# Optimization experiments

Hardware: AMD Instinct MI355X
Metric: run time of the kernel (lower is better)

## Reference

```python
import jax, jax.numpy as jnp
import numpy as np

B, T, HID = 2, 2048, 2048
NH, NKV, HD = 16, 4, 128
GROUPS = NH // NKV

def _rotate_half(t):
    t1, t2 = jnp.split(t, 2, axis=-1)
    return jnp.concatenate([-t2, t1], axis=-1)

def _apply_rotary(t, cos, sin):
    # t: [B, H, T, D], cos/sin: [1, 1, T, D]
    return t * cos + _rotate_half(t) * sin

def setup_inputs() -> dict:
    key = jax.random.key(0)
    ks = jax.random.split(key, 6)
    x = jax.random.normal(ks[0], (B, T, HID), dtype=jnp.float32)
    # real rotary tables
    inv_freq = 1.0 / (10000.0 ** (jnp.arange(0, HD, 2, dtype=jnp.float32) / HD))
    pos = jnp.arange(T, dtype=jnp.float32)
    freqs = jnp.outer(pos, inv_freq)            # [T, D/2]
    emb = jnp.concatenate([freqs, freqs], -1)   # [T, D]
    cos = jnp.cos(emb)[None, None]              # [1,1,T,D]
    sin = jnp.sin(emb)[None, None]
    s = 0.02
    Wq = jax.random.normal(ks[1], (HID, NH * HD), dtype=jnp.float32) * s
    Wk = jax.random.normal(ks[2], (HID, NKV * HD), dtype=jnp.float32) * s
    Wv = jax.random.normal(ks[3], (HID, NKV * HD), dtype=jnp.float32) * s
    Wo = jax.random.normal(ks[4], (NH * HD, HID), dtype=jnp.float32) * s
    return {"x": x, "cos": cos, "sin": sin, "Wq": Wq, "Wk": Wk, "Wv": Wv, "Wo": Wo}

def reference(x, cos, sin, Wq, Wk, Wv, Wo):
    b, t, _ = x.shape
    q = (x @ Wq).reshape(b, t, NH, HD).transpose(0, 2, 1, 3)    # [B,NH,T,D]
    k = (x @ Wk).reshape(b, t, NKV, HD).transpose(0, 2, 1, 3)   # [B,NKV,T,D]
    v = (x @ Wv).reshape(b, t, NKV, HD).transpose(0, 2, 1, 3)
    q = _apply_rotary(q, cos, sin)
    k = _apply_rotary(k, cos, sin)
    # GQA without repeat_interleave: group q-heads by kv-head
    qg = q.reshape(b, NKV, GROUPS, t, HD)                       # [B,KV,G,T,D]
    scale = 1.0 / jnp.sqrt(jnp.float32(HD))
    scores = jnp.einsum('bkgtd,bksd->bkgts', qg, k) * scale     # [B,KV,G,T,S]
    causal = jnp.tril(jnp.ones((t, t), dtype=bool))
    scores = jnp.where(causal[None, None, None], scores, jnp.float32(-1e30))
    attn = jax.nn.softmax(scores, axis=-1)
    out = jnp.einsum('bkgts,bksd->bkgtd', attn, v)              # [B,KV,G,T,D]
    out = out.reshape(b, NH, t, HD).transpose(0, 2, 1, 3).reshape(b, t, NH * HD)
    return out @ Wo
```

## Files before the change

### kernel.cpp

```cpp
#include <hip/hip_runtime.h>
#include <hip/hip_bf16.h>
#include <cstdint>

typedef unsigned short u16;
typedef unsigned int u32;
typedef __bf16 bf16x8 __attribute__((ext_vector_type(8)));
typedef float f32x4 __attribute__((ext_vector_type(4)));

#define BDIM 2
#define TDIM 2048
#define HIDDIM 2048
#define NHEAD 16
#define NKVH 4
#define HD 128
#define MROWS (BDIM*TDIM)
#define NQKV 3072
#define KDIM 2048

#define MFMA16(a,b,c) __builtin_amdgcn_mfma_f32_16x16x32_bf16((a),(b),(c),0,0,0)

__device__ __forceinline__ u16 f2bf(float f) {
    __bf16 h = (__bf16)f;
    return __builtin_bit_cast(u16, h);
}
__device__ __forceinline__ float bf2f(u32 u) {
    u <<= 16;
    return __builtin_bit_cast(float, u);
}
__device__ __forceinline__ void gld16(const void* g, void* l) {
    __builtin_amdgcn_global_load_lds(
        (const __attribute__((address_space(1))) u32*)g,
        (__attribute__((address_space(3))) u32*)l, 16, 0, 0);
}

__global__ __launch_bounds__(256) void cvt_x_kernel(const float* __restrict__ x,
                                                    u16* __restrict__ o) {
    size_t i = ((size_t)blockIdx.x * 256 + threadIdx.x) * 8;
    float4 a = *(const float4*)(x + i);
    float4 b = *(const float4*)(x + i + 4);
    uint4 v;
    v.x = (u32)f2bf(a.x) | ((u32)f2bf(a.y) << 16);
    v.y = (u32)f2bf(a.z) | ((u32)f2bf(a.w) << 16);
    v.z = (u32)f2bf(b.x) | ((u32)f2bf(b.y) << 16);
    v.w = (u32)f2bf(b.z) | ((u32)f2bf(b.w) << 16);
    *(uint4*)(o + i) = v;
}

__global__ __launch_bounds__(256) void transpose_cvt(const float* __restrict__ src,
                                                     u16* __restrict__ dst, int N) {
    __shared__ float tile[32][33];
    int tx = threadIdx.x, ty = threadIdx.y;
    int n0 = blockIdx.x * 32, k0 = blockIdx.y * 32;
#pragma unroll
    for (int r = 0; r < 4; r++)
        tile[ty + 8*r][tx] = src[(size_t)(k0 + ty + 8*r) * N + n0 + tx];
    __syncthreads();
#pragma unroll
    for (int r = 0; r < 4; r++)
        dst[(size_t)(n0 + ty + 8*r) * KDIM + k0 + tx] = f2bf(tile[tx][ty + 8*r]);
}

template<int OUT_BF16>
__global__ void __launch_bounds__(256, 2) gemm_bt(const u16* __restrict__ A,
                                                  const u16* __restrict__ Bt,
                                                  void* __restrict__ C, int ldc) {
    __shared__ __align__(16) u16 Al[128 * 32];
    __shared__ __align__(16) u16 Bl[128 * 32];
    const int tid = threadIdx.x;
    const int lane = tid & 63;
    const int w = tid >> 6;
    const int wm = (w & 1) * 64;
    const int wn = (w >> 1) * 64;
    const int quad = lane >> 4;
    const int l15 = lane & 15;
    const size_t bm = (size_t)blockIdx.x * 128;
    const size_t bn = (size_t)blockIdx.y * 128;

    const int srow = lane >> 2;
    const int kq = (lane & 3) ^ ((lane >> 3) & 3);
    const int i0 = 2 * w, i1 = 2 * w + 1;

    const u16* ga0 = A + (bm + i0*16 + srow) * KDIM + kq * 8;
    const u16* ga1 = A + (bm + i1*16 + srow) * KDIM + kq * 8;
    const u16* gb0 = Bt + (bn + i0*16 + srow) * KDIM + kq * 8;
    const u16* gb1 = Bt + (bn + i1*16 + srow) * KDIM + kq * 8;

    const int swz = ((quad ^ ((l15 >> 1) & 3)) << 3);
    int aoff[4], boff[4];
#pragma unroll
    for (int t = 0; t < 4; t++) {
        aoff[t] = (wm + t*16 + l15) * 32 + swz;
        boff[t] = (wn + t*16 + l15) * 32 + swz;
    }

    f32x4 acc[4][4] = {};

    for (int kt = 0; kt < KDIM / 32; kt++) {
        gld16(ga0 + kt*32, &Al[i0 * 512]);
        gld16(ga1 + kt*32, &Al[i1 * 512]);
        gld16(gb0 + kt*32, &Bl[i0 * 512]);
        gld16(gb1 + kt*32, &Bl[i1 * 512]);
        __syncthreads();
        bf16x8 af[4], bfv[4];
#pragma unroll
        for (int t = 0; t < 4; t++) {
            af[t]  = *(const bf16x8*)&Al[aoff[t]];
            bfv[t] = *(const bf16x8*)&Bl[boff[t]];
        }
#pragma unroll
        for (int mt = 0; mt < 4; mt++)
#pragma unroll
            for (int nt = 0; nt < 4; nt++)
                acc[mt][nt] = MFMA16(af[mt], bfv[nt], acc[mt][nt]);
        __syncthreads();
    }

#pragma unroll
    for (int mt = 0; mt < 4; mt++) {
        size_t m0 = bm + wm + mt*16 + quad*4;
#pragma unroll
        for (int nt = 0; nt < 4; nt++) {
            size_t n = bn + wn + nt*16 + l15;
#pragma unroll
            for (int r = 0; r < 4; r++) {
                if (OUT_BF16)
                    ((u16*)C)[(m0 + r) * (size_t)ldc + n] = f2bf(acc[mt][nt][r]);
                else
                    ((float*)C)[(m0 + r) * (size_t)ldc + n] = acc[mt][nt][r];
            }
        }
    }
}

__global__ __launch_bounds__(256) void rotary_kernel(u16* __restrict__ QKV,
                                                     const float* __restrict__ cosT,
                                                     const float* __restrict__ sinT) {
    int i = blockIdx.x * 256 + threadIdx.x;
    int m = i / 320;
    int rem = i - m * 320;
    int head = rem >> 4;
    int d0 = (rem & 15) << 2;
    int t = m & (TDIM - 1);
    int col;
    float sc;
    if (head < NHEAD) {
        col = head * HD + d0;
        sc = 0.08838834764831845f * 1.4426950408889634f;
    } else {
        col = HIDDIM + (head - NHEAD) * HD + d0;
        sc = 1.0f;
    }
    u16* p0 = QKV + (size_t)m * NQKV + col;
    u16* p1 = p0 + 64;
    float4 cv = *(const float4*)(cosT + t * HD + d0);
    float4 sv = *(const float4*)(sinT + t * HD + d0);
    uint2 qa = *(const uint2*)p0;
    uint2 qb = *(const uint2*)p1;
    float f0[4] = { bf2f(qa.x & 0xffffu), bf2f(qa.x >> 16), bf2f(qa.y & 0xffffu), bf2f(qa.y >> 16) };
    float f1[4] = { bf2f(qb.x & 0xffffu), bf2f(qb.x >> 16), bf2f(qb.y & 0xffffu), bf2f(qb.y >> 16) };
    float c[4] = { cv.x, cv.y, cv.z, cv.w };
    float s[4] = { sv.x, sv.y, sv.z, sv.w };
    u16 o0[4], o1[4];
#pragma unroll
    for (int k = 0; k < 4; k++) {
        o0[k] = f2bf((f0[k] * c[k] - f1[k] * s[k]) * sc);
        o1[k] = f2bf((f1[k] * c[k] + f0[k] * s[k]) * sc);
    }
    uint2 w0, w1;
    w0.x = (u32)o0[0] | ((u32)o0[1] << 16);
    w0.y = (u32)o0[2] | ((u32)o0[3] << 16);
    w1.x = (u32)o1[0] | ((u32)o1[1] << 16);
    w1.y = (u32)o1[2] | ((u32)o1[3] << 16);
    *(uint2*)p0 = w0;
    *(uint2*)p1 = w1;
}

__global__ void __launch_bounds__(256, 2) attn_kernel(const u16* __restrict__ QKV,
                                                      u16* __restrict__ AO) {
    constexpr int LP = 72;
    __shared__ __align__(16) u16 Kl[2][64 * 128];
    __shared__ __align__(16) u16 Vt[128 * 64];
    __shared__ __align__(16) u16 Pl[64 * LP];

    const int pa = blockIdx.x;
    const int h  = blockIdx.y;
    const int b  = blockIdx.z;
    const int kh = h >> 2;
    const int tid = threadIdx.x;
    const int lane = tid & 63;
    const int w = tid >> 6;
    const int quad = lane >> 4;
    const int l15 = lane & 15;

    const size_t rowbase = (size_t)b * TDIM;
    const u16* Qb = QKV + rowbase * NQKV + h * HD;
    const u16* Kb = QKV + rowbase * NQKV + HIDDIM + kh * HD;
    const u16* Vb = Kb + NKVH * HD;

    int krow[4], kgch[4];
#pragma unroll
    for (int i = 0; i < 4; i++) {
        krow[i] = w*16 + i*4 + quad;
        kgch[i] = l15 ^ (krow[i] & 7);
    }
    const int sp0 = tid & 31, dch0 = tid >> 5;
    const int sp1 = sp0, dch1 = dch0 + 8;
    const int vq0 = quad ^ (l15 >> 3);

#pragma unroll 1
    for (int ph = 0; ph < 2; ph++) {
        const int qt = ph ? (31 - pa) : pa;

        bf16x8 qf[4];
        {
            const u16* qr = Qb + (size_t)(qt*64 + w*16 + l15) * NQKV;
#pragma unroll
            for (int kt = 0; kt < 4; kt++)
                qf[kt] = *(const bf16x8*)(qr + kt*32 + quad*8);
        }
        f32x4 O[8] = {};
        float mrun[4], lrun[4];
#pragma unroll
        for (int r = 0; r < 4; r++) { mrun[r] = -1e30f; lrun[r] = 0.0f; }

#pragma unroll
        for (int i = 0; i < 4; i++)
            gld16(Kb + (size_t)krow[i] * NQKV + kgch[i]*8, &Kl[0][(w*16 + i*4) * 128]);
        uint4 vr0a, vr0b, vr1a, vr1b;
        {
            const u16* g0 = Vb + (size_t)(sp0*2) * NQKV + dch0*8;
            vr0a = *(const uint4*)g0;
            vr0b = *(const uint4*)(g0 + NQKV);
            const u16* g1 = Vb + (size_t)(sp1*2) * NQKV + dch1*8;
            vr1a = *(const uint4*)g1;
            vr1b = *(const uint4*)(g1 + NQKV);
        }

#pragma unroll 1
        for (int j = 0; j <= qt; j++) {
            {
                u32 ra[4] = { vr0a.x, vr0a.y, vr0a.z, vr0a.w };
                u32 rb[4] = { vr0b.x, vr0b.y, vr0b.z, vr0b.w };
                int sx = (sp0*2) ^ ((dch0 & 3) << 3);
                int d0 = dch0 * 8;
#pragma unroll
                for (int k2 = 0; k2 < 4; k2++) {
                    u32 lo = (ra[k2] & 0xffffu) | (rb[k2] << 16);
                    u32 hi = (ra[k2] >> 16) | (rb[k2] & 0xffff0000u);
                    *(u32*)&Vt[(d0 + 2*k2)     * 64 + sx] = lo;
                    *(u32*)&Vt[(d0 + 2*k2 + 1) * 64 + sx] = hi;
                }
                u32 rc[4] = { vr1a.x, vr1a.y, vr1a.z, vr1a.w };
                u32 rd[4] = { vr1b.x, vr1b.y, vr1b.z, vr1b.w };
                sx = (sp1*2) ^ ((dch1 & 3) << 3);
                d0 = dch1 * 8;
#pragma unroll
                for (int k2 = 0; k2 < 4; k2++) {
                    u32 lo = (rc[k2] & 0xffffu) | (rd[k2] << 16);
                    u32 hi = (rc[k2] >> 16) | (rd[k2] & 0xffff0000u);
                    *(u32*)&Vt[(d0 + 2*k2)     * 64 + sx] = lo;
                    *(u32*)&Vt[(d0 + 2*k2 + 1) * 64 + sx] = hi;
                }
            }
            __syncthreads();

            if (j < qt) {
                const u16* Kbn = Kb + (size_t)(j+1) * 64 * NQKV;
                u16* kl = Kl[(j+1) & 1];
#pragma unroll
                for (int i = 0; i < 4; i++)
                    gld16(Kbn + (size_t)krow[i] * NQKV + kgch[i]*8, &kl[(w*16 + i*4) * 128]);
                const u16* Vbn = Vb + (size_t)(j+1) * 64 * NQKV;
                const u16* g0 = Vbn + (size_t)(sp0*2) * NQKV + dch0*8;
                vr0a = *(const uint4*)g0;
                vr0b = *(const uint4*)(g0 + NQKV);
                const u16* g1 = Vbn + (size_t)(sp1*2) * NQKV + dch1*8;
                vr1a = *(const uint4*)g1;
                vr1b = *(const uint4*)(g1 + NQKV);
            }

            const u16* kl = Kl[j & 1];
            f32x4 S[4] = {};
#pragma unroll
            for (int kt = 0; kt < 4; kt++) {
                int p = (kt*4 + quad) ^ (l15 & 7);
#pragma unroll
                for (int nt = 0; nt < 4; nt++) {
                    bf16x8 bfr = *(const bf16x8*)&kl[(nt*16 + l15)*128 + p*8];
                    S[nt] = MFMA16(qf[kt], bfr, S[nt]);
                }
            }

            if (j == qt) {
                int toff = w*16 + quad*4;
#pragma unroll
                for (int nt = 0; nt < 4; nt++) {
                    int scol = nt*16 + l15;
#pragma unroll
                    for (int r = 0; r < 4; r++)
                        if (scol > toff + r) S[nt][r] = -1e30f;
                }
            }

            float alpha[4];
#pragma unroll
            for (int r = 0; r < 4; r++) {
                float mx = fmaxf(fmaxf(S[0][r], S[1][r]), fmaxf(S[2][r], S[3][r]));
                mx = fmaxf(mx, __shfl_xor(mx, 1));
                mx = fmaxf(mx, __shfl_xor(mx, 2));
                mx = fmaxf(mx, __shfl_xor(mx, 4));
                mx = fmaxf(mx, __shfl_xor(mx, 8));
                float mnew = fmaxf(mrun[r], mx);
                float al = __builtin_amdgcn_exp2f(mrun[r] - mnew);
                mrun[r] = mnew;
                alpha[r] = al;
                float rs = 0.0f;
#pragma unroll
                for (int nt = 0; nt < 4; nt++) {
                    float p = __builtin_amdgcn_exp2f(S[nt][r] - mnew);
                    S[nt][r] = p;
                    rs += p;
                }
                rs += __shfl_xor(rs, 1);
                rs += __shfl_xor(rs, 2);
                rs += __shfl_xor(rs, 4);
                rs += __shfl_xor(rs, 8);
                lrun[r] = lrun[r] * al + rs;
            }
            bool need = (alpha[0] < 1.0f) | (alpha[1] < 1.0f) |
                        (alpha[2] < 1.0f) | (alpha[3] < 1.0f);
            if (__any(need)) {
#pragma unroll
                for (int nt = 0; nt < 8; nt++)
#pragma unroll
                    for (int r = 0; r < 4; r++)
                        O[nt][r] *= alpha[r];
            }

#pragma unroll
            for (int nt = 0; nt < 4; nt++)
#pragma unroll
                for (int r = 0; r < 4; r++)
                    Pl[(w*16 + quad*4 + r) * LP + nt*16 + l15] = f2bf(S[nt][r]);

#pragma unroll
            for (int kt = 0; kt < 2; kt++) {
                bf16x8 pa_f = *(const bf16x8*)&Pl[(w*16 + l15) * LP + kt*32 + quad*8];
#pragma unroll
                for (int nt = 0; nt < 8; nt++) {
                    int qp = vq0 ^ ((nt & 1) << 1);
                    bf16x8 bv = *(const bf16x8*)&Vt[(nt*16 + l15) * 64 + kt*32 + qp*8];
                    O[nt] = MFMA16(pa_f, bv, O[nt]);
                }
            }
            __syncthreads();
        }

        float inv[4];
#pragma unroll
        for (int r = 0; r < 4; r++) inv[r] = 1.0f / lrun[r];
        size_t row0 = rowbase + qt*64 + w*16 + quad*4;
#pragma unroll
        for (int nt = 0; nt < 8; nt++) {
            size_t cix = (size_t)h * HD + nt*16 + l15;
#pragma unroll
            for (int r = 0; r < 4; r++)
                AO[(row0 + r) * HIDDIM + cix] = f2bf(O[nt][r] * inv[r]);
        }
    }
}

extern "C" void kernel_launch(void* const* d_in, const int* in_sizes, int n_in,
                              void* d_out, int out_size, void* d_ws, size_t ws_size,
                              hipStream_t stream) {
    (void)in_sizes; (void)n_in; (void)out_size; (void)ws_size;
    const float* x    = (const float*)d_in[0];
    const float* cosT = (const float*)d_in[1];
    const float* sinT = (const float*)d_in[2];
    const float* Wq   = (const float*)d_in[3];
    const float* Wk   = (const float*)d_in[4];
    const float* Wv   = (const float*)d_in[5];
    const float* Wo   = (const float*)d_in[6];

    char* ws = (char*)d_ws;
    u16* QKV   = (u16*)ws;
    u16* xb    = (u16*)(ws + (size_t)MROWS * NQKV * 2);
    u16* Wqkvt = (u16*)(ws + (size_t)MROWS * NQKV * 2 + (size_t)MROWS * HIDDIM * 2);
    u16* Wot   = Wqkvt + (size_t)NQKV * KDIM;

    cvt_x_kernel<<<4096, 256, 0, stream>>>(x, xb);
    dim3 tb(32, 8);
    transpose_cvt<<<dim3(64, 64), tb, 0, stream>>>(Wq, Wqkvt, 2048);
    transpose_cvt<<<dim3(16, 64), tb, 0, stream>>>(Wk, Wqkvt + (size_t)2048 * KDIM, 512);
    transpose_cvt<<<dim3(16, 64), tb, 0, stream>>>(Wv, Wqkvt + (size_t)2560 * KDIM, 512);
    transpose_cvt<<<dim3(64, 64), tb, 0, stream>>>(Wo, Wot, 2048);

    gemm_bt<1><<<dim3(32, 24), 256, 0, stream>>>(xb, Wqkvt, QKV, NQKV);
    rotary_kernel<<<5120, 256, 0, stream>>>(QKV, cosT, sinT);
    attn_kernel<<<dim3(16, 16, 2), 256, 0, stream>>>(QKV, xb);
    gemm_bt<0><<<dim3(32, 16), 256, 0, stream>>>(xb, Wot, d_out, HIDDIM);
}
```

Before: 343.3 us.

## Merge prep kernels into one launch, use DPP row reductions, pad V tile

Merges the x conversion and the four weight transpose-convert launches into a single prep kernel dispatched by block index, which removes launch overhead and inter-kernel gaps. In attention, the softmax max and sum reductions switch from shfl_xor to DPP row_ror operations. The transposed V tile drops its XOR swizzle in favour of row padding to 72 elements, which adds a little LDS use and may change bank-conflict behaviour.

```diff
diff --git a/kernel.cpp b/kernel.cpp
--- a/kernel.cpp
+++ b/kernel.cpp
@@ -33,24 +33,67 @@
         (__attribute__((address_space(3))) u32*)l, 16, 0, 0);
 }
 
-__global__ __launch_bounds__(256) void cvt_x_kernel(const float* __restrict__ x,
-                                                    u16* __restrict__ o) {
-    size_t i = ((size_t)blockIdx.x * 256 + threadIdx.x) * 8;
-    float4 a = *(const float4*)(x + i);
-    float4 b = *(const float4*)(x + i + 4);
-    uint4 v;
-    v.x = (u32)f2bf(a.x) | ((u32)f2bf(a.y) << 16);
-    v.y = (u32)f2bf(a.z) | ((u32)f2bf(a.w) << 16);
-    v.z = (u32)f2bf(b.x) | ((u32)f2bf(b.y) << 16);
-    v.w = (u32)f2bf(b.z) | ((u32)f2bf(b.w) << 16);
-    *(uint4*)(o + i) = v;
-}
-
-__global__ __launch_bounds__(256) void transpose_cvt(const float* __restrict__ src,
-                                                     u16* __restrict__ dst, int N) {
+template<int CTRL>
+__device__ __forceinline__ float dpp_rot(float x) {
+    return __builtin_bit_cast(float,
+        __builtin_amdgcn_update_dpp(0, __builtin_bit_cast(int, x),
+                                    CTRL, 0xf, 0xf, true));
+}
+__device__ __forceinline__ float rowmax16(float x) {
+    x = fmaxf(x, dpp_rot<0x121>(x));
+    x = fmaxf(x, dpp_rot<0x122>(x));
+    x = fmaxf(x, dpp_rot<0x124>(x));
+    x = fmaxf(x, dpp_rot<0x128>(x));
+    return x;
+}
+__device__ __forceinline__ float rowsum16(float x) {
+    x += dpp_rot<0x121>(x);
+    x += dpp_rot<0x122>(x);
+    x += dpp_rot<0x124>(x);
+    x += dpp_rot<0x128>(x);
+    return x;
+}
+
+__global__ __launch_bounds__(256) void prep_kernel(const float* __restrict__ x,
+                                                   u16* __restrict__ xb,
+                                                   const float* __restrict__ Wq,
+                                                   const float* __restrict__ Wk,
+                                                   const float* __restrict__ Wv,
+                                                   const float* __restrict__ Wo,
+                                                   u16* __restrict__ Wqkvt,
+                                                   u16* __restrict__ Wot) {
     __shared__ float tile[32][33];
-    int tx = threadIdx.x, ty = threadIdx.y;
-    int n0 = blockIdx.x * 32, k0 = blockIdx.y * 32;
+    const int bi = blockIdx.x;
+    const int tid = threadIdx.x;
+    if (bi < 4096) {
+        size_t i = ((size_t)bi * 256 + tid) * 8;
+        float4 a = *(const float4*)(x + i);
+        float4 b = *(const float4*)(x + i + 4);
+        uint4 v;
+        v.x = (u32)f2bf(a.x) | ((u32)f2bf(a.y) << 16);
+        v.y = (u32)f2bf(a.z) | ((u32)f2bf(a.w) << 16);
+        v.z = (u32)f2bf(b.x) | ((u32)f2bf(b.y) << 16);
+        v.w = (u32)f2bf(b.z) | ((u32)f2bf(b.w) << 16);
+        *(uint4*)(xb + i) = v;
+        return;
+    }
+    const float* src;
+    u16* dst;
+    int N, n0, k0;
+    if (bi < 8192) {
+        int t = bi - 4096; src = Wq; dst = Wqkvt; N = 2048;
+        n0 = (t & 63) * 32; k0 = (t >> 6) * 32;
+    } else if (bi < 9216) {
+        int t = bi - 8192; src = Wk; dst = Wqkvt + (size_t)2048 * KDIM; N = 512;
+        n0 = (t & 15) * 32; k0 = (t >> 4) * 32;
+    } else if (bi < 10240) {
+        int t = bi - 9216; src = Wv; dst = Wqkvt + (size_t)2560 * KDIM; N = 512;
+        n0 = (t & 15) * 32; k0 = (t >> 4) * 32;
+    } else {
+        int t = bi - 10240; src = Wo; dst = Wot; N = 2048;
+        n0 = (t & 63) * 32; k0 = (t >> 6) * 32;
+    }
+    const int tx = tid & 31, ty = tid >> 5;
 #pragma unroll
     for (int r = 0; r < 4; r++)
         tile[ty + 8*r][tx] = src[(size_t)(k0 + ty + 8*r) * N + n0 + tx];
@@ -177,9 +220,10 @@
 
 __global__ void __launch_bounds__(256, 2) attn_kernel(const u16* __restrict__ QKV,
                                                       u16* __restrict__ AO) {
+    constexpr int LV = 72;
     constexpr int LP = 72;
     __shared__ __align__(16) u16 Kl[2][64 * 128];
-    __shared__ __align__(16) u16 Vt[128 * 64];
+    __shared__ __align__(16) u16 Vt[128 * LV];
     __shared__ __align__(16) u16 Pl[64 * LP];
 
     const int pa = blockIdx.x;
@@ -203,9 +247,7 @@
         krow[i] = w*16 + i*4 + quad;
         kgch[i] = l15 ^ (krow[i] & 7);
     }
-    const int sp0 = tid & 31, dch0 = tid >> 5;
-    const int sp1 = sp0, dch1 = dch0 + 8;
-    const int vq0 = quad ^ (l15 >> 3);
+    const int sp0 = tid & 31, dch0 = tid >> 5, dch1 = dch0 + 8;
 
 #pragma unroll 1
     for (int ph = 0; ph < 2; ph++) {
@@ -231,7 +273,7 @@
             const u16* g0 = Vb + (size_t)(sp0*2) * NQKV + dch0*8;
             vr0a = *(const uint4*)g0;
             vr0b = *(const uint4*)(g0 + NQKV);
-            const u16* g1 = Vb + (size_t)(sp1*2) * NQKV + dch1*8;
+            const u16* g1 = Vb + (size_t)(sp0*2) * NQKV + dch1*8;
             vr1a = *(const uint4*)g1;
             vr1b = *(const uint4*)(g1 + NQKV);
         }
@@ -241,25 +283,23 @@
             {
                 u32 ra[4] = { vr0a.x, vr0a.y, vr0a.z, vr0a.w };
                 u32 rb[4] = { vr0b.x, vr0b.y, vr0b.z, vr0b.w };
-                int sx = (sp0*2) ^ ((dch0 & 3) << 3);
-                int d0 = dch0 * 8;
+                int s = sp0*2, d0 = dch0*8;
 #pragma unroll
                 for (int k2 = 0; k2 < 4; k2++) {
                     u32 lo = (ra[k2] & 0xffffu) | (rb[k2] << 16);
                     u32 hi = (ra[k2] >> 16) | (rb[k2] & 0xffff0000u);
-                    *(u32*)&Vt[(d0 + 2*k2)     * 64 + sx] = lo;
-                    *(u32*)&Vt[(d0 + 2*k2 + 1) * 64 + sx] = hi;
+                    *(u32*)&Vt[(d0 + 2*k2)     * LV + s] = lo;
+                    *(u32*)&Vt[(d0 + 2*k2 + 1) * LV + s] = hi;
                 }
                 u32 rc[4] = { vr1a.x, vr1a.y, vr1a.z, vr1a.w };
                 u32 rd[4] = { vr1b.x, vr1b.y, vr1b.z, vr1b.w };
-                sx = (sp1*2) ^ ((dch1 & 3) << 3);
-                d0 = dch1 * 8;
+                d0 = dch1*8;
 #pragma unroll
                 for (int k2 = 0; k2 < 4; k2++) {
                     u32 lo = (rc[k2] & 0xffffu) | (rd[k2] << 16);
                     u32 hi = (rc[k2] >> 16) | (rd[k2] & 0xffff0000u);
-                    *(u32*)&Vt[(d0 + 2*k2)     * 64 + sx] = lo;
-                    *(u32*)&Vt[(d0 + 2*k2 + 1) * 64 + sx] = hi;
+                    *(u32*)&Vt[(d0 + 2*k2)     * LV + s] = lo;
+                    *(u32*)&Vt[(d0 + 2*k2 + 1) * LV + s] = hi;
                 }
             }
             __syncthreads();
@@ -274,7 +314,7 @@
                 const u16* g0 = Vbn + (size_t)(sp0*2) * NQKV + dch0*8;
                 vr0a = *(const uint4*)g0;
                 vr0b = *(const uint4*)(g0 + NQKV);
-                const u16* g1 = Vbn + (size_t)(sp1*2) * NQKV + dch1*8;
+                const u16* g1 = Vbn + (size_t)(sp0*2) * NQKV + dch1*8;
                 vr1a = *(const uint4*)g1;
                 vr1b = *(const uint4*)(g1 + NQKV);
             }
@@ -306,10 +346,7 @@
 #pragma unroll
             for (int r = 0; r < 4; r++) {
                 float mx = fmaxf(fmaxf(S[0][r], S[1][r]), fmaxf(S[2][r], S[3][r]));
-                mx = fmaxf(mx, __shfl_xor(mx, 1));
-                mx = fmaxf(mx, __shfl_xor(mx, 2));
-                mx = fmaxf(mx, __shfl_xor(mx, 4));
-                mx = fmaxf(mx, __shfl_xor(mx, 8));
+                mx = rowmax16(mx);
                 float mnew = fmaxf(mrun[r], mx);
                 float al = __builtin_amdgcn_exp2f(mrun[r] - mnew);
                 mrun[r] = mnew;
@@ -321,10 +358,7 @@
                     S[nt][r] = p;
                     rs += p;
                 }
-                rs += __shfl_xor(rs, 1);
-                rs += __shfl_xor(rs, 2);
-                rs += __shfl_xor(rs, 4);
-                rs += __shfl_xor(rs, 8);
+                rs = rowsum16(rs);
                 lrun[r] = lrun[r] * al + rs;
             }
             bool need = (alpha[0] < 1.0f) | (alpha[1] < 1.0f) |
@@ -348,8 +382,7 @@
                 bf16x8 pa_f = *(const bf16x8*)&Pl[(w*16 + l15) * LP + kt*32 + quad*8];
 #pragma unroll
                 for (int nt = 0; nt < 8; nt++) {
-                    int qp = vq0 ^ ((nt & 1) << 1);
-                    bf16x8 bv = *(const bf16x8*)&Vt[(nt*16 + l15) * 64 + kt*32 + qp*8];
+                    bf16x8 bv = *(const bf16x8*)&Vt[(nt*16 + l15) * LV + kt*32 + quad*8];
                     O[nt] = MFMA16(pa_f, bv, O[nt]);
                 }
             }
@@ -388,13 +421,7 @@
     u16* Wqkvt = (u16*)(ws + (size_t)MROWS * NQKV * 2 + (size_t)MROWS * HIDDIM * 2);
     u16* Wot   = Wqkvt + (size_t)NQKV * KDIM;
 
-    cvt_x_kernel<<<4096, 256, 0, stream>>>(x, xb);
-    dim3 tb(32, 8);
-    transpose_cvt<<<dim3(64, 64), tb, 0, stream>>>(Wq, Wqkvt, 2048);
-    transpose_cvt<<<dim3(16, 64), tb, 0, stream>>>(Wk, Wqkvt + (size_t)2048 * KDIM, 512);
-    transpose_cvt<<<dim3(16, 64), tb, 0, stream>>>(Wv, Wqkvt + (size_t)2560 * KDIM, 512);
-    transpose_cvt<<<dim3(64, 64), tb, 0, stream>>>(Wo, Wot, 2048);
-
+    prep_kernel<<<14336, 256, 0, stream>>>(x, xb, Wq, Wk, Wv, Wo, Wqkvt, Wot);
     gemm_bt<1><<<dim3(32, 24), 256, 0, stream>>>(xb, Wqkvt, QKV, NQKV);
     rotary_kernel<<<5120, 256, 0, stream>>>(QKV, cosT, sinT);
     attn_kernel<<<dim3(16, 16, 2), 256, 0, stream>>>(QKV, xb);
```

Result: faster. 309.3 us (-9.9%).
